# Optimization experiments

Hardware: AMD Instinct MI355X
Metric: run time of the kernel (lower is better)

Reference implementation:

```python
import jax, jax.numpy as jnp
import numpy as np

B, S, D, H = 1, 3072, 2048, 16
HD = D // H          # head_dim = 128
C = HD // 2          # rotary complex pairs = 64
EPS = 1e-6
WINDOW = 3           # frames of sliding-window attention on each side
L_TOKENS = 256       # tokens per frame (forward arg L)
NUM_FRAMES = S // L_TOKENS


def setup_inputs() -> dict:
    key = jax.random.key(0)
    ks = jax.random.split(key, 5)
    scale = 1.0 / np.sqrt(D)
    x = jax.random.normal(ks[0], (B, S, D), jnp.float32)
    wq = jax.random.normal(ks[1], (D, D), jnp.float32) * scale
    wk = jax.random.normal(ks[2], (D, D), jnp.float32) * scale
    wv = jax.random.normal(ks[3], (D, D), jnp.float32) * scale
    wo = jax.random.normal(ks[4], (D, D), jnp.float32) * scale
    bq = jnp.zeros((D,), jnp.float32)
    bk = jnp.zeros((D,), jnp.float32)
    bv = jnp.zeros((D,), jnp.float32)
    bo = jnp.zeros((D,), jnp.float32)
    gq = jnp.ones((D,), jnp.float32)
    gk = jnp.ones((D,), jnp.float32)
    # rotary freqs as cos/sin of angle t * theta_c (source uses a complex [S,1,C] tensor)
    t = jnp.arange(S, dtype=jnp.float32)
    inv_freq = 1.0 / (10000.0 ** (jnp.arange(C, dtype=jnp.float32) / C))
    ang = t[:, None] * inv_freq[None, :]        # [S, C]
    cos = jnp.cos(ang)[:, None, :]              # [S, 1, C]
    sin = jnp.sin(ang)[:, None, :]              # [S, 1, C]
    return {"x": x, "wq": wq, "bq": bq, "wk": wk, "bk": bk, "wv": wv,
            "bv": bv, "wo": wo, "bo": bo, "gq": gq, "gk": gk,
            "cos": cos, "sin": sin, "f": NUM_FRAMES, "L": L_TOKENS}


def _rms_norm(h, g, eps=EPS):
    # tensor_parallel_rms_norm with tp_size=1: fp32 variance, rsqrt, scale by weight
    hf = h.astype(jnp.float32)
    var = jnp.mean(hf * hf, axis=-1, keepdims=True)
    return (hf * jax.lax.rsqrt(var + eps) * g).astype(h.dtype)


def _rope(h, cos, sin):
    # complex rotation on interleaved (real, imag) pairs per head (rope_apply_for3d)
    b, s, d = h.shape
    hd = 2 * cos.shape[-1]
    n = d // hd
    hr = h.reshape(b, s, n, hd)
    xr, xi = hr[..., 0::2], hr[..., 1::2]       # [b,s,n,C]
    c, sn = cos[None], sin[None]                # [1,s,1,C] broadcast over heads
    yr = xr * c - xi * sn
    yi = xr * sn + xi * c
    y = jnp.stack([yr, yi], axis=-1).reshape(b, s, n, hd)
    return y.reshape(b, s, d)


def reference(x, wq, bq, wk, bk, wv, bv, wo, bo, gq, gk, cos, sin, f, L):
    q = _rope(_rms_norm(x @ wq.T + bq, gq), cos, sin)
    k = _rope(_rms_norm(x @ wk.T + bk, gk), cos, sin)
    v = x @ wv.T + bv
    b, s, d = q.shape
    hd = 2 * cos.shape[-1]
    n = d // hd
    qh = q.reshape(b, s, n, hd)
    kh = k.reshape(b, s, n, hd)
    vh = v.reshape(b, s, n, hd)
    scale = 1.0 / np.sqrt(hd)
    scores = jnp.einsum('bqnd,bknd->bnqk', qh, kh) * scale
    win = L * WINDOW
    idx = jnp.arange(s)
    delta = idx[None, :] - idx[:, None]
    mask = (delta <= win) & (delta >= -win)
    scores = jnp.where(mask[None, None], scores, -jnp.inf)
    probs = jax.nn.softmax(scores, axis=-1)
    out = jnp.einsum('bnqk,bknd->bqnd', probs, vh).reshape(b, s, d)
    return out @ wo.T + bo
```

## Files before the change

### kernel.cpp

```cpp
#include <hip/hip_runtime.h>
#include <stdint.h>

typedef unsigned short u16;
typedef __attribute__((ext_vector_type(8))) short short8;
typedef __attribute__((ext_vector_type(4))) float f32x4;

#define S_LEN 3072
#define D_DIM 2048
#define WIN 768
#define INV_SQRT_HD 0.08838834764831845f
#define M_SHIFT 12.0f

__device__ __forceinline__ u16 f2bf(float x) {
  union { float f; uint32_t u; } v; v.f = x;
  uint32_t r = v.u + 0x7FFFu + ((v.u >> 16) & 1u);
  return (u16)(r >> 16);
}
__device__ __forceinline__ float bf2f(u16 x) {
  union { uint32_t u; float f; } v; v.u = ((uint32_t)x) << 16;
  return v.f;
}

__device__ __forceinline__ void load_lds16(const void* g, void* l) {
  __builtin_amdgcn_global_load_lds(
      (const __attribute__((address_space(1))) void*)g,
      (__attribute__((address_space(3))) void*)l, 16, 0, 0);
}

#define MFMA16(a, b, c) __builtin_amdgcn_mfma_f32_16x16x32_bf16((a), (b), (c), 0, 0, 0)

__global__ __launch_bounds__(256) void k_cvt(const float* __restrict__ in,
                                             u16* __restrict__ out, int n4) {
  int i = blockIdx.x * 256 + threadIdx.x;
  if (i >= n4) return;
  float4 v = ((const float4*)in)[i];
  ushort4 o;
  o.x = f2bf(v.x); o.y = f2bf(v.y); o.z = f2bf(v.z); o.w = f2bf(v.w);
  ((ushort4*)out)[i] = o;
}

__global__ __launch_bounds__(256) void k_cvt_w(const float* __restrict__ w0, const float* __restrict__ w1,
                                               const float* __restrict__ w2, const float* __restrict__ w3,
                                               u16* __restrict__ o0, u16* __restrict__ o1,
                                               u16* __restrict__ o2, u16* __restrict__ o3, int n4each) {
  int i = blockIdx.x * 256 + threadIdx.x;
  int seg = i / n4each, off = i - seg * n4each;
  const float* in = seg == 0 ? w0 : seg == 1 ? w1 : seg == 2 ? w2 : w3;
  u16* out = seg == 0 ? o0 : seg == 1 ? o1 : seg == 2 ? o2 : o3;
  float4 v = ((const float4*)in)[off];
  ushort4 o;
  o.x = f2bf(v.x); o.y = f2bf(v.y); o.z = f2bf(v.z); o.w = f2bf(v.w);
  ((ushort4*)out)[off] = o;
}

__device__ __forceinline__ void gemm_body(const u16* __restrict__ A, const u16* __restrict__ B,
                                          int m0, int n0, int t, f32x4 (*acc)[4],
                                          u16* lA, u16* lB) {
  const int lane = t & 63, w = t >> 6, lo = lane & 15, g = lane >> 4;
  const int wr = w >> 1, wc = w & 1;
  const int srow = t >> 2;
  const int sch = (t & 3) ^ ((srow ^ (srow >> 3)) & 3);
  const u16* ga = A + (size_t)(m0 + srow) * D_DIM + sch * 8;
  const u16* gb = B + (size_t)(n0 + srow) * D_DIM + sch * 8;
  for (int k0 = 0; k0 < D_DIM; k0 += 32) {
    load_lds16(ga + k0, &lA[t * 8]);
    load_lds16(ga + (size_t)64 * D_DIM + k0, &lA[2048 + t * 8]);
    load_lds16(gb + k0, &lB[t * 8]);
    load_lds16(gb + (size_t)64 * D_DIM + k0, &lB[2048 + t * 8]);
    __syncthreads();
    short8 af[4], bfr[4];
#pragma unroll
    for (int m = 0; m < 4; ++m) {
      const int R = wr * 64 + m * 16 + lo;
      af[m] = *(const short8*)&lA[R * 32 + ((g ^ ((R ^ (R >> 3)) & 3)) << 3)];
    }
#pragma unroll
    for (int n = 0; n < 4; ++n) {
      const int R = wc * 64 + n * 16 + lo;
      bfr[n] = *(const short8*)&lB[R * 32 + ((g ^ ((R ^ (R >> 3)) & 3)) << 3)];
    }
#pragma unroll
    for (int m = 0; m < 4; ++m)
#pragma unroll
      for (int n = 0; n < 4; ++n) acc[m][n] = MFMA16(af[m], bfr[n], acc[m][n]);
    __syncthreads();
  }
}

__global__ __launch_bounds__(256) void k_gemm_qkv(const u16* __restrict__ A,
                                                  const u16* __restrict__ Bq, const u16* __restrict__ Bk,
                                                  const u16* __restrict__ Bv,
                                                  const float* __restrict__ bq, const float* __restrict__ bk,
                                                  const float* __restrict__ bv,
                                                  float* __restrict__ Q0, float* __restrict__ K0,
                                                  u16* __restrict__ Vb) {
  __shared__ u16 lA[128 * 32];
  __shared__ u16 lB[128 * 32];
  const int id = blockIdx.x;
  const int swz = (id & 7) * 144 + (id >> 3);
  const int bx = swz / 24, by = swz % 24;
  const int n0g = bx * 128, m0 = by * 128;
  const int seg = n0g >> 11, n0 = n0g & 2047;
  const u16* B = seg == 0 ? Bq : seg == 1 ? Bk : Bv;
  const float* bias = seg == 0 ? bq : seg == 1 ? bk : bv;
  const int t = threadIdx.x;
  const int lane = t & 63, w = t >> 6, lo = lane & 15, g = lane >> 4;
  const int wr = w >> 1, wc = w & 1;
  const f32x4 zero4 = {0.f, 0.f, 0.f, 0.f};
  f32x4 acc[4][4];
#pragma unroll
  for (int m = 0; m < 4; ++m)
#pragma unroll
    for (int n = 0; n < 4; ++n) acc[m][n] = zero4;
  gemm_body(A, B, m0, n0, t, acc, lA, lB);
#pragma unroll
  for (int m = 0; m < 4; ++m) {
    const int row = m0 + wr * 64 + m * 16 + 4 * g;
#pragma unroll
    for (int n = 0; n < 4; ++n) {
      const int col = n0 + wc * 64 + n * 16 + lo;
      const float bb = bias[col];
#pragma unroll
      for (int r = 0; r < 4; ++r) {
        const float val = acc[m][n][r] + bb;
        if (seg == 2)
          Vb[(size_t)(row + r) * 2048 + col] = f2bf(val);
        else if (seg == 1)
          K0[(size_t)(row + r) * 2048 + col] = val;
        else
          Q0[(size_t)(row + r) * 2048 + col] = val;
      }
    }
  }
}

template <bool BF16OUT>
__global__ __launch_bounds__(256) void k_gemm_nt(const u16* __restrict__ A,
                                                 const u16* __restrict__ B,
                                                 const float* __restrict__ bias,
                                                 void* __restrict__ Cv, int nby) {
  __shared__ u16 lA[128 * 32];
  __shared__ u16 lB[128 * 32];
  const int id = blockIdx.x;
  const int cpx = gridDim.x >> 3;
  const int swz = (id & 7) * cpx + (id >> 3);
  const int bx = swz / nby, by = swz % nby;
  const int n0 = bx * 128, m0 = by * 128;
  const int t = threadIdx.x;
  const int lane = t & 63, w = t >> 6, lo = lane & 15, g = lane >> 4;
  const int wr = w >> 1, wc = w & 1;
  const f32x4 zero4 = {0.f, 0.f, 0.f, 0.f};
  f32x4 acc[4][4];
#pragma unroll
  for (int m = 0; m < 4; ++m)
#pragma unroll
    for (int n = 0; n < 4; ++n) acc[m][n] = zero4;
  gemm_body(A, B, m0, n0, t, acc, lA, lB);
#pragma unroll
  for (int m = 0; m < 4; ++m) {
    const int row = m0 + wr * 64 + m * 16 + 4 * g;
#pragma unroll
    for (int n = 0; n < 4; ++n) {
      const int col = n0 + wc * 64 + n * 16 + lo;
      const float bb = bias[col];
#pragma unroll
      for (int r = 0; r < 4; ++r) {
        const float val = acc[m][n][r] + bb;
        if (BF16OUT)
          ((u16*)Cv)[(size_t)(row + r) * 2048 + col] = f2bf(val);
        else
          ((float*)Cv)[(size_t)(row + r) * 2048 + col] = val;
      }
    }
  }
}

__global__ __launch_bounds__(256) void k_rms_rope(const float* __restrict__ H,
                                                  const float* __restrict__ gain,
                                                  const float* __restrict__ cosT,
                                                  const float* __restrict__ sinT,
                                                  u16* __restrict__ out) {
  const int s = blockIdx.x, t = threadIdx.x;
  const float* hp = H + (size_t)s * D_DIM + t * 8;
  float4 v0 = *(const float4*)hp;
  float4 v1 = *(const float4*)(hp + 4);
  float h[8] = {v0.x, v0.y, v0.z, v0.w, v1.x, v1.y, v1.z, v1.w};
  float ss = 0.f;
#pragma unroll
  for (int j = 0; j < 8; ++j) ss += h[j] * h[j];
#pragma unroll
  for (int off = 32; off > 0; off >>= 1) ss += __shfl_xor(ss, off);
  __shared__ float red[4];
  if ((t & 63) == 0) red[t >> 6] = ss;
  __syncthreads();
  ss = red[0] + red[1] + red[2] + red[3];
  const float rs = rsqrtf(ss * (1.f / D_DIM) + 1e-6f);
  const float4 g0 = *(const float4*)(gain + t * 8);
  const float4 g1 = *(const float4*)(gain + t * 8 + 4);
  float y[8];
  y[0] = h[0] * rs * g0.x; y[1] = h[1] * rs * g0.y;
  y[2] = h[2] * rs * g0.z; y[3] = h[3] * rs * g0.w;
  y[4] = h[4] * rs * g1.x; y[5] = h[5] * rs * g1.y;
  y[6] = h[6] * rs * g1.z; y[7] = h[7] * rs * g1.w;
  const int cbase = ((t * 8) & 127) >> 1;
  short8 o8;
#pragma unroll
  for (int i = 0; i < 4; ++i) {
    const float cs = cosT[s * 64 + cbase + i];
    const float sn = sinT[s * 64 + cbase + i];
    const float yr = y[2 * i] * cs - y[2 * i + 1] * sn;
    const float yi = y[2 * i] * sn + y[2 * i + 1] * cs;
    o8[2 * i] = (short)f2bf(yr);
    o8[2 * i + 1] = (short)f2bf(yi);
  }
  *(short8*)(out + (size_t)s * D_DIM + t * 8) = o8;
}

__global__ __launch_bounds__(256) void k_transpose(const u16* __restrict__ in,
                                                   u16* __restrict__ out) {
  __shared__ u16 tile[64][72];
  const int s0 = blockIdx.x * 64, d0 = blockIdx.y * 64;
  const int t = threadIdx.x;
  const int r = t >> 3, c8 = (t & 7) * 8;
#pragma unroll
  for (int p = 0; p < 2; ++p) {
    short8 v = *(const short8*)&in[(size_t)(s0 + r + p * 32) * D_DIM + d0 + c8];
#pragma unroll
    for (int j = 0; j < 8; ++j) tile[r + p * 32][c8 + j] = (u16)v[j];
  }
  __syncthreads();
#pragma unroll
  for (int p = 0; p < 2; ++p) {
    const int dr = r + p * 32;
    short8 o;
#pragma unroll
    for (int j = 0; j < 8; ++j) o[j] = (short)tile[c8 + j][dr];
    *(short8*)&out[(size_t)(d0 + dr) * S_LEN + s0 + c8] = o;
  }
}

__global__ __launch_bounds__(256, 3) void k_attn5(const u16* __restrict__ Q,
                                                  const u16* __restrict__ Kmat,
                                                  const u16* __restrict__ Vt,
                                                  u16* __restrict__ Oa,
                                                  u16* __restrict__ Ob,
                                                  float* __restrict__ lbuf) {
  const int qt = blockIdx.x, h = blockIdx.y, z = blockIdx.z;
  const int t = threadIdx.x, w = t >> 6, lane = t & 63, lo = lane & 15, g = lane >> 4;
  const int q0 = qt * 128;
  const int wrow = q0 + w * 32;
  const size_t hoff = (size_t)h * 128;

  __shared__ u16 lK[2][32 * 128];
  __shared__ u16 lV[2][128 * 32];
  __shared__ u16 ldsp[4][32][40];

  short8 qf[2][4];
#pragma unroll
  for (int m = 0; m < 2; ++m) {
    const u16* qp = Q + (size_t)(wrow + m * 16 + lo) * D_DIM + hoff + g * 8;
#pragma unroll
    for (int c = 0; c < 4; ++c) qf[m][c] = *(const short8*)(qp + c * 32);
  }

  const f32x4 zero4 = {0.f, 0.f, 0.f, 0.f};
  f32x4 oacc[2][8];
#pragma unroll
  for (int m = 0; m < 2; ++m)
#pragma unroll
    for (int ct = 0; ct < 8; ++ct) oacc[m][ct] = zero4;
  float lrun[2][4] = {{0.f, 0.f, 0.f, 0.f}, {0.f, 0.f, 0.f, 0.f}};

  int jlo = q0 - WIN; if (jlo < 0) jlo = 0;
  int jhi = q0 + 127 + WIN + 1; if (jhi > S_LEN) jhi = S_LEN;
  const int NT = (jhi - jlo) >> 5;
  const int it0 = z * (NT >> 1), it1 = it0 + (NT >> 1);

  const int krow = t >> 4,         kch  = (t & 15) ^ (krow & 7);
  const int krow1 = (t + 256) >> 4, kch1 = (t & 15) ^ (krow1 & 7);
  const int vrow = t >> 2,         vch  = (t & 3) ^ ((vrow >> 1) & 3);
  const int vrow1 = (t + 256) >> 2, vch1 = (t & 3) ^ ((vrow1 >> 1) & 3);

#define STAGE5(buf, jj)                                                                              \
  do {                                                                                               \
    load_lds16(Kmat + (size_t)((jj) + krow) * D_DIM + hoff + (kch << 3), &lK[buf][t * 8]);           \
    load_lds16(Kmat + (size_t)((jj) + krow1) * D_DIM + hoff + (kch1 << 3), &lK[buf][(t + 256) * 8]); \
    load_lds16(Vt + (size_t)(hoff + vrow) * S_LEN + (jj) + (vch << 3), &lV[buf][t * 8]);             \
    load_lds16(Vt + (size_t)(hoff + vrow1) * S_LEN + (jj) + (vch1 << 3), &lV[buf][(t + 256) * 8]);   \
  } while (0)

  STAGE5(0, jlo + (it0 << 5));
  __syncthreads();
  int cur = 0;
  for (int it = it0; it < it1; ++it) {
    const int j0 = jlo + (it << 5);
    if (it + 1 < it1) STAGE5(cur ^ 1, j0 + 32);

    f32x4 sc[2][2];
    sc[0][0] = zero4; sc[0][1] = zero4; sc[1][0] = zero4; sc[1][1] = zero4;
#pragma unroll
    for (int half = 0; half < 2; ++half) {
#pragma unroll
      for (int c = 0; c < 4; ++c) {
        const short8 kf = *(const short8*)
            &lK[cur][(half * 16 + lo) * 128 + (((g + 4 * c) ^ (lo & 7)) << 3)];
        sc[0][half] = MFMA16(qf[0][c], kf, sc[0][half]);
        sc[1][half] = MFMA16(qf[1][c], kf, sc[1][half]);
      }
    }

    const int dq = j0 - q0;
    const bool interior = (dq >= -640) && (dq <= 736);
#pragma unroll
    for (int m = 0; m < 2; ++m) {
#pragma unroll
      for (int r = 0; r < 4; ++r) {
        float a0 = fmaf(sc[m][0][r], INV_SQRT_HD, -M_SHIFT);
        float a1 = fmaf(sc[m][1][r], INV_SQRT_HD, -M_SHIFT);
        if (!interior) {
          const int dk = j0 + lo - (wrow + m * 16 + 4 * g + r);
          if (dk < -WIN || dk > WIN) a0 = -3e38f;
          if (dk + 16 < -WIN || dk + 16 > WIN) a1 = -3e38f;
        }
        const float p0 = __expf(a0);
        const float p1 = __expf(a1);
        lrun[m][r] += p0 + p1;
        ldsp[w][m * 16 + 4 * g + r][lo] = f2bf(p0);
        ldsp[w][m * 16 + 4 * g + r][16 + lo] = f2bf(p1);
      }
    }

    const short8 pf0 = *(const short8*)&ldsp[w][lo][g * 8];
    const short8 pf1 = *(const short8*)&ldsp[w][16 + lo][g * 8];
#pragma unroll
    for (int ct = 0; ct < 8; ++ct) {
      const short8 vf = *(const short8*)
          &lV[cur][(ct * 16 + lo) * 32 + ((g ^ ((lo >> 1) & 3)) << 3)];
      oacc[0][ct] = MFMA16(pf0, vf, oacc[0][ct]);
      oacc[1][ct] = MFMA16(pf1, vf, oacc[1][ct]);
    }
    __syncthreads();
    cur ^= 1;
  }
#undef STAGE5

#pragma unroll
  for (int off = 8; off > 0; off >>= 1)
#pragma unroll
    for (int m = 0; m < 2; ++m)
#pragma unroll
      for (int r = 0; r < 4; ++r) lrun[m][r] += __shfl_xor(lrun[m][r], off);

  u16* Op = z ? Ob : Oa;
#pragma unroll
  for (int m = 0; m < 2; ++m)
#pragma unroll
    for (int r = 0; r < 4; ++r) {
      const int row = wrow + m * 16 + 4 * g + r;
#pragma unroll
      for (int ct = 0; ct < 8; ++ct)
        Op[(size_t)row * D_DIM + hoff + ct * 16 + lo] = f2bf(oacc[m][ct][r]);
      if (lo == 0) lbuf[(size_t)z * S_LEN * 16 + (size_t)row * 16 + h] = lrun[m][r];
    }
}

__global__ __launch_bounds__(256) void k_combine(const u16* __restrict__ Oa,
                                                 const u16* __restrict__ Ob,
                                                 const float* __restrict__ lbuf,
                                                 u16* __restrict__ out) {
  const int i = blockIdx.x * 256 + threadIdx.x;
  const int s = i >> 8, d8 = (i & 255) * 8, h = d8 >> 7;
  const float la = lbuf[(size_t)s * 16 + h];
  const float lb = lbuf[(size_t)S_LEN * 16 + (size_t)s * 16 + h];
  const float inv = 1.f / (la + lb);
  const size_t base = (size_t)s * D_DIM + d8;
  const short8 a = *(const short8*)(Oa + base);
  const short8 b = *(const short8*)(Ob + base);
  short8 o;
#pragma unroll
  for (int j = 0; j < 8; ++j)
    o[j] = (short)f2bf((bf2f((u16)a[j]) + bf2f((u16)b[j])) * inv);
  *(short8*)(out + base) = o;
}

extern "C" void kernel_launch(void* const* d_in, const int* in_sizes, int n_in,
                              void* d_out, int out_size, void* d_ws, size_t ws_size,
                              hipStream_t stream) {
  const float* x    = (const float*)d_in[0];
  const float* wq   = (const float*)d_in[1];
  const float* bq   = (const float*)d_in[2];
  const float* wk   = (const float*)d_in[3];
  const float* bk   = (const float*)d_in[4];
  const float* wv   = (const float*)d_in[5];
  const float* bv   = (const float*)d_in[6];
  const float* wo   = (const float*)d_in[7];
  const float* bo   = (const float*)d_in[8];
  const float* gq   = (const float*)d_in[9];
  const float* gk   = (const float*)d_in[10];
  const float* cosT = (const float*)d_in[11];
  const float* sinT = (const float*)d_in[12];

  char* ws = (char*)d_ws;
  const size_t WB = (size_t)D_DIM * D_DIM * 2;
  const size_t XB = (size_t)S_LEN * D_DIM * 2;
  const size_t XF = (size_t)S_LEN * D_DIM * 4;
  u16*   wq_bf = (u16*)(ws);
  u16*   wk_bf = (u16*)(ws + WB);
  u16*   wv_bf = (u16*)(ws + 2 * WB);
  u16*   wo_bf = (u16*)(ws + 3 * WB);
  u16*   x_bf  = (u16*)(ws + 4 * WB);
  float* Q0    = (float*)(ws + 4 * WB + XB);
  float* K0    = (float*)(ws + 4 * WB + XB + XF);
  u16*   V0b   = (u16*)(ws + 4 * WB + XB + 2 * XF);
  float* lbuf  = (float*)(ws + 4 * WB + 2 * XB + 2 * XF);
  u16* q_bf = x_bf;
  u16* k_bf = wq_bf;
  u16* vT   = (u16*)Q0;
  u16* Ob   = (u16*)K0;
  u16* Oa   = (u16*)d_out;
  u16* attn = V0b;

  const int nw4 = (D_DIM * D_DIM) / 4;
  const int nx4 = (S_LEN * D_DIM) / 4;
  k_cvt<<<nx4 / 256, 256, 0, stream>>>(x, x_bf, nx4);
  k_cvt_w<<<4 * nw4 / 256, 256, 0, stream>>>(wq, wk, wv, wo, wq_bf, wk_bf, wv_bf, wo_bf, nw4);

  k_gemm_qkv<<<1152, 256, 0, stream>>>(x_bf, wq_bf, wk_bf, wv_bf, bq, bk, bv, Q0, K0, V0b);

  k_rms_rope<<<S_LEN, 256, 0, stream>>>(Q0, gq, cosT, sinT, q_bf);
  k_rms_rope<<<S_LEN, 256, 0, stream>>>(K0, gk, cosT, sinT, k_bf);
  k_transpose<<<dim3(S_LEN / 64, D_DIM / 64), 256, 0, stream>>>(V0b, vT);

  k_attn5<<<dim3(S_LEN / 128, 16, 2), 256, 0, stream>>>(q_bf, k_bf, vT, Oa, Ob, lbuf);
  k_combine<<<(S_LEN * D_DIM / 8) / 256, 256, 0, stream>>>(Oa, Ob, lbuf, attn);

  k_gemm_nt<false><<<384, 256, 0, stream>>>(attn, wo_bf, bo, (float*)d_out, 24);
}
```

Before: 272.4 us.

## Replace QKV GEMM with 256x256 double-buffered tile kernel and bf16 Q/K outputs

Replaces the 128x128, single-buffered QKV projection GEMM with a 256x256-tile, 512-thread kernel. The new kernel double-buffers 64-wide K slices in LDS, uses an XOR-swizzled layout, and raises wave priority around the MFMA bursts. Q and K pre-norm outputs are now stored as bf16 instead of fp32, which halves that intermediate traffic, and the RMS-norm/rope kernel reads bf16. The aim is higher operand reuse and load/compute overlap in the dominant GEMM. The cost is more LDS (128KB per block), fewer blocks (288) for the GPU's CUs, and extra rounding of Q/K before normalisation.

After: 281.0 us. +3.2%, slower.

```diff
diff --git a/kernel.cpp b/kernel.cpp
--- a/kernel.cpp
+++ b/kernel.cpp
@@ -51,6 +51,122 @@
   ushort4 o;
   o.x = f2bf(v.x); o.y = f2bf(v.y); o.z = f2bf(v.z); o.w = f2bf(v.w);
   ((ushort4*)out)[off] = o;
+}
+
+__global__ __launch_bounds__(512, 2) void k_g256(const u16* __restrict__ A,
+                                                 const u16* __restrict__ Bq, const u16* __restrict__ Bk,
+                                                 const u16* __restrict__ Bv,
+                                                 const float* __restrict__ bq, const float* __restrict__ bk,
+                                                 const float* __restrict__ bv,
+                                                 u16* __restrict__ Qb, u16* __restrict__ Kb,
+                                                 u16* __restrict__ Vb) {
+  __shared__ u16 lds[2][4][128 * 64];
+
+  const int id = blockIdx.x;
+  const int swz = (id & 7) * 36 + (id >> 3);
+  const int bx = swz / 12, by = swz % 12;
+  const int m0 = by * 256;
+  const int seg = bx >> 3;
+  const int n0 = (bx & 7) * 256;
+  const u16* B = seg == 0 ? Bq : seg == 1 ? Bk : Bv;
+  const float* bias = seg == 0 ? bq : seg == 1 ? bk : bv;
+  u16* D = seg == 0 ? Qb : seg == 1 ? Kb : Vb;
+
+  const int t = threadIdx.x;
+  const int w = t >> 6, wm = w >> 2, wn = w & 3;
+  const int lane = t & 63, lo = lane & 15, g = lane >> 4;
+
+  const int srow = t >> 3;
+  const int csrc = (t & 7) ^ (srow & 7);
+  const u16* gA = A + (size_t)(m0 + srow) * D_DIM + csrc * 8;
+  const u16* gB = B + (size_t)(n0 + srow) * D_DIM + csrc * 8;
+
+#define STG(buf, k0)                                                            \
+  do {                                                                          \
+    load_lds16(gA + (k0),                      &lds[buf][0][t * 8]);            \
+    load_lds16(gA + (size_t)64 * D_DIM + (k0), &lds[buf][0][4096 + t * 8]);     \
+    load_lds16(gA + (size_t)128 * D_DIM + (k0), &lds[buf][1][t * 8]);           \
+    load_lds16(gA + (size_t)192 * D_DIM + (k0), &lds[buf][1][4096 + t * 8]);    \
+    load_lds16(gB + (k0),                      &lds[buf][2][t * 8]);            \
+    load_lds16(gB + (size_t)64 * D_DIM + (k0), &lds[buf][2][4096 + t * 8]);     \
+    load_lds16(gB + (size_t)128 * D_DIM + (k0), &lds[buf][3][t * 8]);           \
+    load_lds16(gB + (size_t)192 * D_DIM + (k0), &lds[buf][3][4096 + t * 8]);    \
+  } while (0)
+
+  const f32x4 zero4 = {0.f, 0.f, 0.f, 0.f};
+  f32x4 acc[8][4];
+#pragma unroll
+  for (int m = 0; m < 8; ++m)
+#pragma unroll
+    for (int n = 0; n < 4; ++n) acc[m][n] = zero4;
+
+  STG(0, 0);
+  int cur = 0;
+  const int NKT = D_DIM / 64;
+  for (int T = 0; T < NKT; ++T) {
+    const int k0n = (T + 1) << 6;
+    if (T + 1 < NKT) {
+      STG(cur ^ 1, k0n);
+      asm volatile("s_waitcnt vmcnt(8)" ::: "memory");
+    } else {
+      asm volatile("s_waitcnt vmcnt(0)" ::: "memory");
+    }
+    __builtin_amdgcn_s_barrier();
+    asm volatile("" ::: "memory");
+
+    const u16* pA = &lds[cur][wm][0];
+    const u16* pB = &lds[cur][2 + (wn >> 1)][0];
+    const int rbb = (wn & 1) * 64;
+
+#pragma unroll
+    for (int ph = 0; ph < 4; ++ph) {
+      const int mb = (ph >> 1) * 4, nb = (ph & 1) * 2;
+      short8 aF[4][2], bF[2][2];
+#pragma unroll
+      for (int i = 0; i < 4; ++i) {
+        const int ra = (mb + i) * 16 + lo;
+#pragma unroll
+        for (int kk = 0; kk < 2; ++kk)
+          aF[i][kk] = *(const short8*)&pA[ra * 64 + ((((kk << 2) + g) ^ (ra & 7)) << 3)];
+      }
+#pragma unroll
+      for (int j = 0; j < 2; ++j) {
+        const int rb = rbb + (nb + j) * 16 + lo;
+#pragma unroll
+        for (int kk = 0; kk < 2; ++kk)
+          bF[j][kk] = *(const short8*)&pB[rb * 64 + ((((kk << 2) + g) ^ (rb & 7)) << 3)];
+      }
+      __builtin_amdgcn_s_setprio(1);
+#pragma unroll
+      for (int i = 0; i < 4; ++i)
+#pragma unroll
+        for (int j = 0; j < 2; ++j)
+#pragma unroll
+          for (int kk = 0; kk < 2; ++kk)
+            acc[mb + i][nb + j] = MFMA16(aF[i][kk], bF[j][kk], acc[mb + i][nb + j]);
+      __builtin_amdgcn_s_setprio(0);
+      __builtin_amdgcn_sched_barrier(0);
+    }
+
+    asm volatile("" ::: "memory");
+    __builtin_amdgcn_s_barrier();
+    asm volatile("" ::: "memory");
+    cur ^= 1;
+  }
+#undef STG
+
+#pragma unroll
+  for (int mf = 0; mf < 8; ++mf) {
+    const int row = m0 + wm * 128 + mf * 16 + 4 * g;
+#pragma unroll
+    for (int nf = 0; nf < 4; ++nf) {
+      const int col = n0 + wn * 64 + nf * 16 + lo;
+      const float bb = bias[col];
+#pragma unroll
+      for (int rr = 0; rr < 4; ++rr)
+        D[(size_t)(row + rr) * D_DIM + col] = f2bf(acc[mf][nf][rr] + bb);
+    }
+  }
 }
 
 __device__ __forceinline__ void gemm_body(const u16* __restrict__ A, const u16* __restrict__ B,
@@ -84,53 +200,6 @@
 #pragma unroll
       for (int n = 0; n < 4; ++n) acc[m][n] = MFMA16(af[m], bfr[n], acc[m][n]);
     __syncthreads();
-  }
-}
-
-__global__ __launch_bounds__(256) void k_gemm_qkv(const u16* __restrict__ A,
-                                                  const u16* __restrict__ Bq, const u16* __restrict__ Bk,
-                                                  const u16* __restrict__ Bv,
-                                                  const float* __restrict__ bq, const float* __restrict__ bk,
-                                                  const float* __restrict__ bv,
-                                                  float* __restrict__ Q0, float* __restrict__ K0,
-                                                  u16* __restrict__ Vb) {
-  __shared__ u16 lA[128 * 32];
-  __shared__ u16 lB[128 * 32];
-  const int id = blockIdx.x;
-  const int swz = (id & 7) * 144 + (id >> 3);
-  const int bx = swz / 24, by = swz % 24;
-  const int n0g = bx * 128, m0 = by * 128;
-  const int seg = n0g >> 11, n0 = n0g & 2047;
-  const u16* B = seg == 0 ? Bq : seg == 1 ? Bk : Bv;
-  const float* bias = seg == 0 ? bq : seg == 1 ? bk : bv;
-  const int t = threadIdx.x;
-  const int lane = t & 63, w = t >> 6, lo = lane & 15, g = lane >> 4;
-  const int wr = w >> 1, wc = w & 1;
-  const f32x4 zero4 = {0.f, 0.f, 0.f, 0.f};
-  f32x4 acc[4][4];
-#pragma unroll
-  for (int m = 0; m < 4; ++m)
-#pragma unroll
-    for (int n = 0; n < 4; ++n) acc[m][n] = zero4;
-  gemm_body(A, B, m0, n0, t, acc, lA, lB);
-#pragma unroll
-  for (int m = 0; m < 4; ++m) {
-    const int row = m0 + wr * 64 + m * 16 + 4 * g;
-#pragma unroll
-    for (int n = 0; n < 4; ++n) {
-      const int col = n0 + wc * 64 + n * 16 + lo;
-      const float bb = bias[col];
-#pragma unroll
-      for (int r = 0; r < 4; ++r) {
-        const float val = acc[m][n][r] + bb;
-        if (seg == 2)
-          Vb[(size_t)(row + r) * 2048 + col] = f2bf(val);
-        else if (seg == 1)
-          K0[(size_t)(row + r) * 2048 + col] = val;
-        else
-          Q0[(size_t)(row + r) * 2048 + col] = val;
-      }
-    }
   }
 }
 
@@ -175,16 +244,16 @@
   }
 }
 
-__global__ __launch_bounds__(256) void k_rms_rope(const float* __restrict__ H,
-                                                  const float* __restrict__ gain,
-                                                  const float* __restrict__ cosT,
-                                                  const float* __restrict__ sinT,
-                                                  u16* __restrict__ out) {
+__global__ __launch_bounds__(256) void k_rms_rope_b(const u16* __restrict__ H,
+                                                    const float* __restrict__ gain,
+                                                    const float* __restrict__ cosT,
+                                                    const float* __restrict__ sinT,
+                                                    u16* __restrict__ out) {
   const int s = blockIdx.x, t = threadIdx.x;
-  const float* hp = H + (size_t)s * D_DIM + t * 8;
-  float4 v0 = *(const float4*)hp;
-  float4 v1 = *(const float4*)(hp + 4);
-  float h[8] = {v0.x, v0.y, v0.z, v0.w, v1.x, v1.y, v1.z, v1.w};
+  const short8 hv = *(const short8*)(H + (size_t)s * D_DIM + t * 8);
+  float h[8];
+#pragma unroll
+  for (int j = 0; j < 8; ++j) h[j] = bf2f((u16)hv[j]);
   float ss = 0.f;
 #pragma unroll
   for (int j = 0; j < 8; ++j) ss += h[j] * h[j];
@@ -276,9 +345,9 @@
   const int NT = (jhi - jlo) >> 5;
   const int it0 = z * (NT >> 1), it1 = it0 + (NT >> 1);
 
-  const int krow = t >> 4,         kch  = (t & 15) ^ (krow & 7);
+  const int krow = t >> 4,          kch  = (t & 15) ^ (krow & 7);
   const int krow1 = (t + 256) >> 4, kch1 = (t & 15) ^ (krow1 & 7);
-  const int vrow = t >> 2,         vch  = (t & 3) ^ ((vrow >> 1) & 3);
+  const int vrow = t >> 2,          vch  = (t & 3) ^ ((vrow >> 1) & 3);
   const int vrow1 = (t + 256) >> 2, vch1 = (t & 3) ^ ((vrow1 >> 1) & 3);
 
 #define STAGE5(buf, jj)                                                                              \
@@ -403,20 +472,19 @@
   char* ws = (char*)d_ws;
   const size_t WB = (size_t)D_DIM * D_DIM * 2;
   const size_t XB = (size_t)S_LEN * D_DIM * 2;
-  const size_t XF = (size_t)S_LEN * D_DIM * 4;
   u16*   wq_bf = (u16*)(ws);
   u16*   wk_bf = (u16*)(ws + WB);
   u16*   wv_bf = (u16*)(ws + 2 * WB);
   u16*   wo_bf = (u16*)(ws + 3 * WB);
   u16*   x_bf  = (u16*)(ws + 4 * WB);
-  float* Q0    = (float*)(ws + 4 * WB + XB);
-  float* K0    = (float*)(ws + 4 * WB + XB + XF);
-  u16*   V0b   = (u16*)(ws + 4 * WB + XB + 2 * XF);
-  float* lbuf  = (float*)(ws + 4 * WB + 2 * XB + 2 * XF);
+  u16*   Q0b   = (u16*)(ws + 4 * WB + XB);
+  u16*   K0b   = (u16*)(ws + 4 * WB + 2 * XB);
+  u16*   V0b   = (u16*)(ws + 4 * WB + 3 * XB);
+  float* lbuf  = (float*)(ws + 4 * WB + 4 * XB);
   u16* q_bf = x_bf;
   u16* k_bf = wq_bf;
-  u16* vT   = (u16*)Q0;
-  u16* Ob   = (u16*)K0;
+  u16* vT   = Q0b;
+  u16* Ob   = K0b;
   u16* Oa   = (u16*)d_out;
   u16* attn = V0b;
 
@@ -425,10 +493,10 @@
   k_cvt<<<nx4 / 256, 256, 0, stream>>>(x, x_bf, nx4);
   k_cvt_w<<<4 * nw4 / 256, 256, 0, stream>>>(wq, wk, wv, wo, wq_bf, wk_bf, wv_bf, wo_bf, nw4);
 
-  k_gemm_qkv<<<1152, 256, 0, stream>>>(x_bf, wq_bf, wk_bf, wv_bf, bq, bk, bv, Q0, K0, V0b);
-
-  k_rms_rope<<<S_LEN, 256, 0, stream>>>(Q0, gq, cosT, sinT, q_bf);
-  k_rms_rope<<<S_LEN, 256, 0, stream>>>(K0, gk, cosT, sinT, k_bf);
+  k_g256<<<288, 512, 0, stream>>>(x_bf, wq_bf, wk_bf, wv_bf, bq, bk, bv, Q0b, K0b, V0b);
+
+  k_rms_rope_b<<<S_LEN, 256, 0, stream>>>(Q0b, gq, cosT, sinT, q_bf);
+  k_rms_rope_b<<<S_LEN, 256, 0, stream>>>(K0b, gk, cosT, sinT, k_bf);
   k_transpose<<<dim3(S_LEN / 64, D_DIM / 64), 256, 0, stream>>>(V0b, vT);
 
   k_attn5<<<dim3(S_LEN / 128, 16, 2), 256, 0, stream>>>(q_bf, k_bf, vT, Oa, Ob, lbuf);
```
